# Kernel tuning notes

Measured on AMD Instinct MI355X. Metric: run time of the kernel, lower is better.

## Reference

```python
import math
import jax, jax.numpy as jnp
import numpy as np

N_HEADS = 32
ALIBI_BIAS_MAX = 8


def _alibi_slopes(n_heads, alibi_bias_max=8):
    _n = 2 ** math.ceil(math.log2(n_heads))
    m = jnp.arange(1, _n + 1, dtype=jnp.float32) * (alibi_bias_max / _n)
    slopes = 1.0 / jnp.power(2.0, m)
    if _n != n_heads:
        slopes = jnp.concatenate([slopes[1::2], slopes[::2]])[:n_heads]
    return slopes  # [H]


def setup_inputs() -> dict:
    key = jax.random.key(0)
    k1, k2, k3 = jax.random.split(key, 3)
    B, S, D = 1, 2048, 4096
    x = jax.random.normal(k1, (B, S, D), dtype=jnp.float32)
    w_qkv = jax.random.normal(k2, (3 * D, D), dtype=jnp.float32) * 0.02
    b_qkv = jnp.zeros((3 * D,), dtype=jnp.float32)
    w_out = jax.random.normal(k3, (D, D), dtype=jnp.float32) * 0.02
    b_out = jnp.zeros((D,), dtype=jnp.float32)
    return {"x": x, "w_qkv": w_qkv, "b_qkv": b_qkv, "w_out": w_out, "b_out": b_out}


def reference(x, w_qkv, b_qkv, w_out, b_out):
    B, S, D = x.shape
    H = N_HEADS
    hd = D // H
    # fused QKV projection (weights stored [Out, In], out_first=True)
    qkv = jnp.einsum("bsd,od->bso", x, w_qkv) + b_qkv  # [B,S,3D]
    q, k, v = jnp.split(qkv, 3, axis=-1)
    q = q.reshape(B, S, H, hd)
    k = k.reshape(B, S, H, hd)
    v = v.reshape(B, S, H, hd)
    scale = 1.0 / math.sqrt(hd)
    scores = jnp.einsum("bqhd,bkhd->bhqk", q, k) * scale  # [B,H,S,S]
    # ALiBi bias: slopes[h] * arange(1-KSeqLen, 1), broadcast over query pos
    slopes = _alibi_slopes(H, ALIBI_BIAS_MAX)  # [H]
    positions = jnp.arange(1 - S, 1, dtype=jnp.float32)  # [S] key positions
    alibi = slopes[:, None] * positions[None, :]  # [H, S_k]
    scores = scores + alibi[None, :, None, :]
    # causal mask
    causal = jnp.arange(S)[:, None] >= jnp.arange(S)[None, :]  # [Sq, Sk]
    scores = jnp.where(causal[None, None, :, :], scores, jnp.float32(-1e9))
    attn = jax.nn.softmax(scores, axis=-1)
    out = jnp.einsum("bhqk,bkhd->bqhd", attn, v).reshape(B, S, D)
    return jnp.einsum("bsd,od->bso", out, w_out) + b_out
```

## Files before the change

kernel.cpp:

```cpp
#include <hip/hip_runtime.h>
#include <hip/hip_bf16.h>

typedef __bf16 bf16;
typedef __attribute__((ext_vector_type(8))) __bf16 bf16x8;
typedef __attribute__((ext_vector_type(4))) float f32x4;

#define GLOAD_LDS16(g, l)                                                        \
    __builtin_amdgcn_global_load_lds(                                            \
        (const __attribute__((address_space(1))) void*)(g),                      \
        (__attribute__((address_space(3))) void*)(l), 16, 0, 0)

#define WAITV(n) asm volatile("s_waitcnt vmcnt(" #n ")" ::: "memory")
#define LGKM0()  asm volatile("s_waitcnt lgkmcnt(0)" ::: "memory")
#define BAR()    __builtin_amdgcn_s_barrier()
#define SCHEDB() __builtin_amdgcn_sched_barrier(0)

__global__ __launch_bounds__(256) void cvt_f32_bf16(
    const float* __restrict__ src, bf16* __restrict__ dst, int n16)
{
    int idx = blockIdx.x * 256 + threadIdx.x;
    const int stride = gridDim.x * 256;
    for (int i = idx; i < n16; i += stride) {
        const float* p = src + (size_t)i * 16;
        f32x4 a = *(const f32x4*)p;
        f32x4 b = *(const f32x4*)(p + 4);
        f32x4 c = *(const f32x4*)(p + 8);
        f32x4 d = *(const f32x4*)(p + 12);
        bf16x8 h0, h1;
#pragma unroll
        for (int j = 0; j < 4; ++j) {
            h0[j] = (bf16)a[j]; h0[4 + j] = (bf16)b[j];
            h1[j] = (bf16)c[j]; h1[4 + j] = (bf16)d[j];
        }
        bf16* q = dst + (size_t)i * 16;
        *(bf16x8*)q = h0;
        *(bf16x8*)(q + 8) = h1;
    }
}

template <int OUT_BF16>
__global__ __launch_bounds__(512, 2) void gemm_sp(
    const bf16* __restrict__ A, const bf16* __restrict__ B,
    const float* __restrict__ bias, void* __restrict__ Cout,
    int K, int ldc, int nbx)
{
    constexpr int ASZ = 128 * 64;
    constexpr int BUF = ASZ + 256 * 64;
    __shared__ bf16 lds[3 * BUF];

    int bx, by;
    if ((nbx & 15) == 0) {
        const int r = (int)blockIdx.x & 255;
        const int slot = r >> 3;
        bx = ((int)blockIdx.x >> 8) * 16 + (r & 7) * 2 + (slot >> 4);
        by = slot & 15;
    } else {
        const int cpx = gridDim.x >> 3;
        const int swz = ((int)blockIdx.x & 7) * cpx + ((int)blockIdx.x >> 3);
        bx = swz % nbx; by = swz / nbx;
    }
    const int brow = by * 128, bcol = bx * 256;

    const int tid  = threadIdx.x;
    const int wv   = tid >> 6, lane = tid & 63;
    const int lo   = lane & 15, hi = lane >> 4;
    const int wrp  = wv >> 2, wcp = wv & 3;

    const int srow = lane >> 3;
    const int scol = ((lane & 7) ^ (lane >> 3)) * 8;

    f32x4 acc[4][4];
#pragma unroll
    for (int m = 0; m < 4; ++m)
#pragma unroll
        for (int n = 0; n < 4; ++n)
            acc[m][n] = (f32x4){0.f, 0.f, 0.f, 0.f};

    auto STAGE = [&](int t) {
        const int k0 = t * 64;
        bf16* lb = &lds[(t % 3) * BUF];
#pragma unroll
        for (int j = 0; j < 2; ++j) {
            const int c = wv * 2 + j;
            GLOAD_LDS16(A + (size_t)(brow + c * 8 + srow) * K + k0 + scol, lb + c * 512);
        }
#pragma unroll
        for (int j = 0; j < 4; ++j) {
            const int c = wv * 4 + j;
            GLOAD_LDS16(B + (size_t)(bcol + c * 8 + srow) * K + k0 + scol, lb + ASZ + c * 512);
        }
    };

    const int nt = K / 64;
    STAGE(0); STAGE(1);
    WAITV(6); BAR(); SCHEDB();

    for (int t = 0; t < nt; ++t) {
        const bf16* lb = &lds[(t % 3) * BUF];
        bf16x8 af[4][2], bfr[4][2];
#pragma unroll
        for (int m = 0; m < 4; ++m) {
            const int ru = wrp * 64 + m * 16 + lo;
#pragma unroll
            for (int kk = 0; kk < 2; ++kk)
                af[m][kk] = *(const bf16x8*)&lb[ru * 64 + (((kk * 4 + hi) ^ (lo & 7)) * 8)];
        }
#pragma unroll
        for (int n = 0; n < 4; ++n) {
            const int rb = wcp * 64 + n * 16 + lo;
#pragma unroll
            for (int kk = 0; kk < 2; ++kk)
                bfr[n][kk] = *(const bf16x8*)&lb[ASZ + rb * 64 + (((kk * 4 + hi) ^ (lo & 7)) * 8)];
        }

        if (t + 2 < nt) STAGE(t + 2);

        __builtin_amdgcn_s_setprio(1);
#pragma unroll
        for (int m = 0; m < 4; ++m)
#pragma unroll
            for (int n = 0; n < 4; ++n)
#pragma unroll
                for (int kk = 0; kk < 2; ++kk)
                    acc[m][n] = __builtin_amdgcn_mfma_f32_16x16x32_bf16(af[m][kk], bfr[n][kk], acc[m][n], 0, 0, 0);
        __builtin_amdgcn_s_setprio(0);

        if (t + 2 < nt)      WAITV(6);
        else if (t + 1 < nt) WAITV(0);
        if (t + 1 < nt) { BAR(); SCHEDB(); }
    }

#pragma unroll
    for (int m = 0; m < 4; ++m) {
        const int row = brow + wrp * 64 + m * 16 + hi * 4;
#pragma unroll
        for (int n = 0; n < 4; ++n) {
            const int col = bcol + wcp * 64 + n * 16 + lo;
            const float bv = bias[col];
#pragma unroll
            for (int r = 0; r < 4; ++r) {
                const float v = acc[m][n][r] + bv;
                if (OUT_BF16)
                    ((bf16*)Cout)[(size_t)(row + r) * ldc + col] = (bf16)v;
                else
                    ((float*)Cout)[(size_t)(row + r) * ldc + col] = v;
            }
        }
    }
}

__global__ __launch_bounds__(512) void attn_mfma(
    const bf16* __restrict__ qkv, bf16* __restrict__ attn_out)
{
    const int S = 2048, QKV = 12288, D = 4096, HD = 128;
    const int bid = blockIdx.x;
    const int h   = bid & 31;
    const int qi  = 15 - (bid >> 5);
    const int q0  = qi * 128;
    const int tid = threadIdx.x;
    const int w    = tid >> 6, lane = tid & 63;
    const int lo   = lane & 15, hi = lane >> 4;
    const int qbase = q0 + w * 16;

    __shared__ bf16 Ks[64 * 128];
    __shared__ bf16 Vs[128 * 72];
    __shared__ bf16 Ps[8 * 16 * 72];

    const float scale = 0.08838834764831845f;
    const float slope = exp2f(-0.25f * (float)(h + 1));

    bf16x8 qfrag[4];
#pragma unroll
    for (int ds = 0; ds < 4; ++ds)
        qfrag[ds] = *(const bf16x8*)(qkv + (size_t)(qbase + lo) * QKV + h * HD + ds * 32 + hi * 8);

    f32x4 o[8];
#pragma unroll
    for (int dt = 0; dt < 8; ++dt) o[dt] = (f32x4){0.f, 0.f, 0.f, 0.f};
    float mrow[4] = {-1e30f, -1e30f, -1e30f, -1e30f};
    float lrow[4] = {0.f, 0.f, 0.f, 0.f};

    const int krow = tid >> 3;
    const int kch  = tid & 7;
    const int vp2  = tid & 63;
    const int voct = tid >> 6;

    bf16x8 kpre0, kpre1;
    unsigned vpre[8];
    auto ISSUE = [&](int t) {
        const int kv0 = t * 64;
        const bf16* kp = qkv + (size_t)(kv0 + krow) * QKV + D + h * HD + kch * 16;
        kpre0 = *(const bf16x8*)kp;
        kpre1 = *(const bf16x8*)(kp + 8);
        const bf16* vp = qkv + (size_t)(kv0 + voct * 8) * QKV + 2 * D + h * HD + 2 * vp2;
#pragma unroll
        for (int j = 0; j < 8; ++j)
            vpre[j] = *(const unsigned*)(vp + (size_t)j * QKV);
    };

    const int ntile = (q0 + 128) / 64;
    ISSUE(0);
    for (int t = 0; t < ntile; ++t) {
        const int kv0 = t * 64;
        {
            const int kb  = krow * 128 + kch * 16;
            const int swzk = (krow & 7) << 3;
            *(bf16x8*)&Ks[kb ^ swzk]       = kpre0;
            *(bf16x8*)&Ks[(kb + 8) ^ swzk] = kpre1;
            bf16x8 r0, r1;
#pragma unroll
            for (int j = 0; j < 8; ++j) {
                unsigned short us0 = (unsigned short)(vpre[j] & 0xffff);
                unsigned short us1 = (unsigned short)(vpre[j] >> 16);
                r0[j] = *(const bf16*)&us0;
                r1[j] = *(const bf16*)&us1;
            }
            *(bf16x8*)&Vs[(2 * vp2) * 72 + voct * 8]     = r0;
            *(bf16x8*)&Vs[(2 * vp2 + 1) * 72 + voct * 8] = r1;
        }
        LGKM0(); BAR(); SCHEDB();

        if (t + 1 < ntile) ISSUE(t + 1);

        if (kv0 <= qbase + 15) {
            f32x4 c[4];
#pragma unroll
            for (int j = 0; j < 4; ++j) c[j] = (f32x4){0.f, 0.f, 0.f, 0.f};
            __builtin_amdgcn_s_setprio(1);
#pragma unroll
            for (int ds = 0; ds < 4; ++ds) {
#pragma unroll
                for (int j = 0; j < 4; ++j) {
                    const int r = j * 16 + lo;
                    bf16x8 b = *(const bf16x8*)&Ks[(r * 128 + ds * 32 + hi * 8) ^ ((r & 7) << 3)];
                    c[j] = __builtin_amdgcn_mfma_f32_16x16x32_bf16(qfrag[ds], b, c[j], 0, 0, 0);
                }
            }
            __builtin_amdgcn_s_setprio(0);
#pragma unroll
            for (int r = 0; r < 4; ++r) {
                const int q = qbase + hi * 4 + r;
                float s[4];
#pragma unroll
                for (int j = 0; j < 4; ++j) {
                    const int ki = kv0 + j * 16 + lo;
                    s[j] = c[j][r] * scale + slope * (float)(ki - (S - 1));
                    if (ki > q) s[j] = -1e30f;
                }
                float tm = fmaxf(fmaxf(s[0], s[1]), fmaxf(s[2], s[3]));
                tm = fmaxf(tm, __shfl_xor(tm, 1));
                tm = fmaxf(tm, __shfl_xor(tm, 2));
                tm = fmaxf(tm, __shfl_xor(tm, 4));
                tm = fmaxf(tm, __shfl_xor(tm, 8));
                const float mnew = fmaxf(mrow[r], tm);
                const float cr = __expf(mrow[r] - mnew);
                float p[4], ps = 0.f;
#pragma unroll
                for (int j = 0; j < 4; ++j) { p[j] = __expf(s[j] - mnew); ps += p[j]; }
                ps += __shfl_xor(ps, 1);
                ps += __shfl_xor(ps, 2);
                ps += __shfl_xor(ps, 4);
                ps += __shfl_xor(ps, 8);
                lrow[r] = lrow[r] * cr + ps;
                mrow[r] = mnew;
#pragma unroll
                for (int dt = 0; dt < 8; ++dt) o[dt][r] *= cr;
#pragma unroll
                for (int j = 0; j < 4; ++j)
                    Ps[w * 1152 + (hi * 4 + r) * 72 + j * 16 + lo] = (bf16)p[j];
            }
            bf16x8 pa0 = *(const bf16x8*)&Ps[w * 1152 + lo * 72 + hi * 8];
            bf16x8 pa1 = *(const bf16x8*)&Ps[w * 1152 + lo * 72 + 32 + hi * 8];
            __builtin_amdgcn_s_setprio(1);
#pragma unroll
            for (int dt = 0; dt < 8; ++dt) {
                bf16x8 bv0 = *(const bf16x8*)&Vs[(dt * 16 + lo) * 72 + hi * 8];
                bf16x8 bv1 = *(const bf16x8*)&Vs[(dt * 16 + lo) * 72 + 32 + hi * 8];
                o[dt] = __builtin_amdgcn_mfma_f32_16x16x32_bf16(pa0, bv0, o[dt], 0, 0, 0);
                o[dt] = __builtin_amdgcn_mfma_f32_16x16x32_bf16(pa1, bv1, o[dt], 0, 0, 0);
            }
            __builtin_amdgcn_s_setprio(0);
        }
        SCHEDB(); BAR(); SCHEDB();
    }

#pragma unroll
    for (int r = 0; r < 4; ++r) {
        const float inv = 1.0f / lrow[r];
        const int q = qbase + hi * 4 + r;
        bf16* op = attn_out + (size_t)q * D + h * HD;
#pragma unroll
        for (int dt = 0; dt < 8; ++dt)
            op[dt * 16 + lo] = (bf16)(o[dt][r] * inv);
    }
}

extern "C" void kernel_launch(void* const* d_in, const int* in_sizes, int n_in,
                              void* d_out, int out_size, void* d_ws, size_t ws_size,
                              hipStream_t stream) {
    const int S = 2048, D = 4096, QKV = 12288;
    const int NH = 6144;
    const float* x     = (const float*)d_in[0];
    const float* w_qkv = (const float*)d_in[1];
    const float* b_qkv = (const float*)d_in[2];
    const float* w_out = (const float*)d_in[3];
    const float* b_out = (const float*)d_in[4];
    float* out = (float*)d_out;

    char* ws = (char*)d_ws;
    const size_t need_full = (size_t)S * D * 2 + (size_t)QKV * D * 2 + (size_t)S * QKV * 2;

    if (ws_size >= need_full) {
        bf16* xb    = (bf16*)ws;
        bf16* attnb = xb;
        bf16* wqb   = (bf16*)(ws + (size_t)S * D * 2);
        bf16* wob   = wqb;
        bf16* qkvb  = (bf16*)(ws + (size_t)S * D * 2 + (size_t)QKV * D * 2);

        cvt_f32_bf16<<<2048, 256, 0, stream>>>(x, xb, S * D / 16);
        cvt_f32_bf16<<<4096, 256, 0, stream>>>(w_qkv, wqb, QKV * D / 16);
        gemm_sp<1><<<(QKV / 256) * (S / 128), 512, 0, stream>>>(xb, wqb, b_qkv, qkvb, D, QKV, QKV / 256);
        attn_mfma<<<512, 512, 0, stream>>>(qkvb, attnb);
        cvt_f32_bf16<<<2048, 256, 0, stream>>>(w_out, wob, D * D / 16);
        gemm_sp<0><<<(D / 256) * (S / 128), 512, 0, stream>>>(attnb, wob, b_out, out, D, D, D / 256);
    } else {
        bf16* xb    = (bf16*)ws;
        bf16* attnb = xb;
        bf16* wb    = (bf16*)(ws + (size_t)S * D * 2);
        bf16* wob   = wb;
        bf16* qkvb  = (bf16*)(ws + (size_t)S * D * 2 + (size_t)NH * D * 2);

        cvt_f32_bf16<<<2048, 256, 0, stream>>>(x, xb, S * D / 16);
        cvt_f32_bf16<<<2048, 256, 0, stream>>>(w_qkv, wb, NH * D / 16);
        gemm_sp<1><<<(NH / 256) * (S / 128), 512, 0, stream>>>(xb, wb, b_qkv, qkvb, D, QKV, NH / 256);
        cvt_f32_bf16<<<2048, 256, 0, stream>>>(w_qkv + (size_t)NH * D, wb, NH * D / 16);
        gemm_sp<1><<<(NH / 256) * (S / 128), 512, 0, stream>>>(xb, wb, b_qkv + NH, qkvb + NH, D, QKV, NH / 256);
        attn_mfma<<<512, 512, 0, stream>>>(qkvb, attnb);
        cvt_f32_bf16<<<2048, 256, 0, stream>>>(w_out, wob, D * D / 16);
        gemm_sp<0><<<(D / 256) * (S / 128), 512, 0, stream>>>(attnb, wob, b_out, out, D, D, D / 256);
    }
}
```

Baseline: 428.3 us.

## Merge conversions, fold w_out conversion into attention, and skip softmax rescaling

Merges the x and w_qkv fp32-to-bf16 conversions into one launch. Appends extra blocks to the attention kernel that convert w_out, so that conversion can overlap attention instead of running as its own kernel. In the online softmax, the max and rescale update is skipped when no row max in the tile exceeds the running max by more than 8. This cuts the exp and accumulator-scaling work, in exchange for exp values up to e^8 before normalization and a warp-uniform branch.

```diff
diff --git a/kernel.cpp b/kernel.cpp
--- a/kernel.cpp
+++ b/kernel.cpp
@@ -14,27 +14,44 @@
 #define LGKM0()  asm volatile("s_waitcnt lgkmcnt(0)" ::: "memory")
 #define BAR()    __builtin_amdgcn_s_barrier()
 #define SCHEDB() __builtin_amdgcn_sched_barrier(0)
+
+__device__ __forceinline__ void cvt16(const float* __restrict__ p, bf16* __restrict__ q) {
+    f32x4 a = *(const f32x4*)p;
+    f32x4 b = *(const f32x4*)(p + 4);
+    f32x4 c = *(const f32x4*)(p + 8);
+    f32x4 d = *(const f32x4*)(p + 12);
+    bf16x8 h0, h1;
+#pragma unroll
+    for (int j = 0; j < 4; ++j) {
+        h0[j] = (bf16)a[j]; h0[4 + j] = (bf16)b[j];
+        h1[j] = (bf16)c[j]; h1[4 + j] = (bf16)d[j];
+    }
+    *(bf16x8*)q = h0;
+    *(bf16x8*)(q + 8) = h1;
+}
 
 __global__ __launch_bounds__(256) void cvt_f32_bf16(
     const float* __restrict__ src, bf16* __restrict__ dst, int n16)
 {
     int idx = blockIdx.x * 256 + threadIdx.x;
     const int stride = gridDim.x * 256;
-    for (int i = idx; i < n16; i += stride) {
-        const float* p = src + (size_t)i * 16;
-        f32x4 a = *(const f32x4*)p;
-        f32x4 b = *(const f32x4*)(p + 4);
-        f32x4 c = *(const f32x4*)(p + 8);
-        f32x4 d = *(const f32x4*)(p + 12);
-        bf16x8 h0, h1;
-#pragma unroll
-        for (int j = 0; j < 4; ++j) {
-            h0[j] = (bf16)a[j]; h0[4 + j] = (bf16)b[j];
-            h1[j] = (bf16)c[j]; h1[4 + j] = (bf16)d[j];
-        }
-        bf16* q = dst + (size_t)i * 16;
-        *(bf16x8*)q = h0;
-        *(bf16x8*)(q + 8) = h1;
+    for (int i = idx; i < n16; i += stride)
+        cvt16(src + (size_t)i * 16, dst + (size_t)i * 16);
+}
+
+__global__ __launch_bounds__(256) void cvt2_f32_bf16(
+    const float* __restrict__ s1, bf16* __restrict__ d1, int n1,
+    const float* __restrict__ s2, bf16* __restrict__ d2, int n2)
+{
+    int idx = blockIdx.x * 256 + threadIdx.x;
+    const int stride = gridDim.x * 256;
+    const int ntot = n1 + n2;
+    for (int i = idx; i < ntot; i += stride) {
+        if (i < n1) cvt16(s1 + (size_t)i * 16, d1 + (size_t)i * 16);
+        else {
+            const int j = i - n1;
+            cvt16(s2 + (size_t)j * 16, d2 + (size_t)j * 16);
+        }
     }
 }
 
@@ -149,9 +166,18 @@
     }
 }
 
-__global__ __launch_bounds__(512) void attn_mfma(
-    const bf16* __restrict__ qkv, bf16* __restrict__ attn_out)
+__global__ __launch_bounds__(512) void attn_cvt(
+    const bf16* __restrict__ qkv, bf16* __restrict__ attn_out,
+    const float* __restrict__ wsrc, bf16* __restrict__ wdst, int n16w)
 {
+    if (blockIdx.x >= 512) {
+        int idx = ((int)blockIdx.x - 512) * 512 + threadIdx.x;
+        const int stride = ((int)gridDim.x - 512) * 512;
+        for (int i = idx; i < n16w; i += stride)
+            cvt16(wsrc + (size_t)i * 16, wdst + (size_t)i * 16);
+        return;
+    }
+
     const int S = 2048, QKV = 12288, D = 4096, HD = 128;
     const int bid = blockIdx.x;
     const int h   = bid & 31;
@@ -252,22 +278,36 @@
                 tm = fmaxf(tm, __shfl_xor(tm, 2));
                 tm = fmaxf(tm, __shfl_xor(tm, 4));
                 tm = fmaxf(tm, __shfl_xor(tm, 8));
-                const float mnew = fmaxf(mrow[r], tm);
-                const float cr = __expf(mrow[r] - mnew);
-                float p[4], ps = 0.f;
-#pragma unroll
-                for (int j = 0; j < 4; ++j) { p[j] = __expf(s[j] - mnew); ps += p[j]; }
-                ps += __shfl_xor(ps, 1);
-                ps += __shfl_xor(ps, 2);
-                ps += __shfl_xor(ps, 4);
-                ps += __shfl_xor(ps, 8);
-                lrow[r] = lrow[r] * cr + ps;
-                mrow[r] = mnew;
-#pragma unroll
-                for (int dt = 0; dt < 8; ++dt) o[dt][r] *= cr;
-#pragma unroll
-                for (int j = 0; j < 4; ++j)
-                    Ps[w * 1152 + (hi * 4 + r) * 72 + j * 16 + lo] = (bf16)p[j];
+                if (__all(tm <= mrow[r] + 8.0f)) {
+                    float p[4], ps = 0.f;
+#pragma unroll
+                    for (int j = 0; j < 4; ++j) { p[j] = __expf(s[j] - mrow[r]); ps += p[j]; }
+                    ps += __shfl_xor(ps, 1);
+                    ps += __shfl_xor(ps, 2);
+                    ps += __shfl_xor(ps, 4);
+                    ps += __shfl_xor(ps, 8);
+                    lrow[r] += ps;
+#pragma unroll
+                    for (int j = 0; j < 4; ++j)
+                        Ps[w * 1152 + (hi * 4 + r) * 72 + j * 16 + lo] = (bf16)p[j];
+                } else {
+                    const float mnew = fmaxf(mrow[r], tm);
+                    const float cr = __expf(mrow[r] - mnew);
+                    float p[4], ps = 0.f;
+#pragma unroll
+                    for (int j = 0; j < 4; ++j) { p[j] = __expf(s[j] - mnew); ps += p[j]; }
+                    ps += __shfl_xor(ps, 1);
+                    ps += __shfl_xor(ps, 2);
+                    ps += __shfl_xor(ps, 4);
+                    ps += __shfl_xor(ps, 8);
+                    lrow[r] = lrow[r] * cr + ps;
+                    mrow[r] = mnew;
+#pragma unroll
+                    for (int dt = 0; dt < 8; ++dt) o[dt][r] *= cr;
+#pragma unroll
+                    for (int j = 0; j < 4; ++j)
+                        Ps[w * 1152 + (hi * 4 + r) * 72 + j * 16 + lo] = (bf16)p[j];
+                }
             }
             bf16x8 pa0 = *(const bf16x8*)&Ps[w * 1152 + lo * 72 + hi * 8];
             bf16x8 pa1 = *(const bf16x8*)&Ps[w * 1152 + lo * 72 + 32 + hi * 8];
@@ -317,11 +357,9 @@
         bf16* wob   = wqb;
         bf16* qkvb  = (bf16*)(ws + (size_t)S * D * 2 + (size_t)QKV * D * 2);
 
-        cvt_f32_bf16<<<2048, 256, 0, stream>>>(x, xb, S * D / 16);
-        cvt_f32_bf16<<<4096, 256, 0, stream>>>(w_qkv, wqb, QKV * D / 16);
+        cvt2_f32_bf16<<<3584, 256, 0, stream>>>(x, xb, S * D / 16, w_qkv, wqb, QKV * D / 16);
         gemm_sp<1><<<(QKV / 256) * (S / 128), 512, 0, stream>>>(xb, wqb, b_qkv, qkvb, D, QKV, QKV / 256);
-        attn_mfma<<<512, 512, 0, stream>>>(qkvb, attnb);
-        cvt_f32_bf16<<<2048, 256, 0, stream>>>(w_out, wob, D * D / 16);
+        attn_cvt<<<1024, 512, 0, stream>>>(qkvb, attnb, w_out, wob, D * D / 16);
         gemm_sp<0><<<(D / 256) * (S / 128), 512, 0, stream>>>(attnb, wob, b_out, out, D, D, D / 256);
     } else {
         bf16* xb    = (bf16*)ws;
@@ -330,13 +368,11 @@
         bf16* wob   = wb;
         bf16* qkvb  = (bf16*)(ws + (size_t)S * D * 2 + (size_t)NH * D * 2);
 
-        cvt_f32_bf16<<<2048, 256, 0, stream>>>(x, xb, S * D / 16);
-        cvt_f32_bf16<<<2048, 256, 0, stream>>>(w_qkv, wb, NH * D / 16);
+        cvt2_f32_bf16<<<3584, 256, 0, stream>>>(x, xb, S * D / 16, w_qkv, wb, NH * D / 16);
         gemm_sp<1><<<(NH / 256) * (S / 128), 512, 0, stream>>>(xb, wb, b_qkv, qkvb, D, QKV, NH / 256);
         cvt_f32_bf16<<<2048, 256, 0, stream>>>(w_qkv + (size_t)NH * D, wb, NH * D / 16);
         gemm_sp<1><<<(NH / 256) * (S / 128), 512, 0, stream>>>(xb, wb, b_qkv + NH, qkvb + NH, D, QKV, NH / 256);
-        attn_mfma<<<512, 512, 0, stream>>>(qkvb, attnb);
-        cvt_f32_bf16<<<2048, 256, 0, stream>>>(w_out, wob, D * D / 16);
+        attn_cvt<<<1024, 512, 0, stream>>>(qkvb, attnb, w_out, wob, D * D / 16);
         gemm_sp<0><<<(D / 256) * (S / 128), 512, 0, stream>>>(attnb, wob, b_out, out, D, D, D / 256);
     }
 }
```

After: 810.3 us. 89.2% more time.
